# Kernel optimization log

Hardware: AMD Instinct MI355X
Metric: run time of the kernel (lower is better)

Reference implementation:

```python
import jax, jax.numpy as jnp
import numpy as np

N, F, FE = 50000, 128, 1
E, EI, G = 800000, 400000, 64
NEG_SLOPE = 0.01


def _linear_params(key, out_dim, in_dim):
    k1, k2 = jax.random.split(key)
    bound = 1.0 / np.sqrt(in_dim)
    w = jax.random.uniform(k1, (out_dim, in_dim), jnp.float32, -bound, bound)
    b = jax.random.uniform(k2, (out_dim,), jnp.float32, -bound, bound)
    return w, b


def setup_inputs() -> dict:
    key = jax.random.key(0)
    ks = jax.random.split(key, 16)
    inp = {
        'x': jax.random.normal(ks[0], (N, F), jnp.float32),
        'edge_index': jax.random.randint(ks[1], (2, E), 0, N, jnp.int64) if jax.config.read('jax_enable_x64') else jax.random.randint(ks[1], (2, E), 0, N, jnp.int32),
        'edge_attr': jax.random.normal(ks[2], (E, FE), jnp.float32),
        'internal_edge_index': jax.random.randint(ks[3], (2, EI), 0, N, jnp.int32),
        'internal_edge_attr': jax.random.normal(ks[4], (EI, FE), jnp.float32),
        'batch': jnp.sort(jax.random.randint(ks[5], (N,), 0, G, jnp.int32)),
    }
    # four conv sub-modules: message Linear(2F+FE -> 1), update Linear(F+1 -> F)
    names = ['e1', 'e2', 'i1', 'i2']
    for i, nm in enumerate(names):
        wm, bm = _linear_params(ks[6 + i], 1, 2 * F + FE)
        wu, bu = _linear_params(ks[10 + i], F, F + 1)
        inp[f'wm_{nm}'], inp[f'bm_{nm}'] = wm, bm
        inp[f'wu_{nm}'], inp[f'bu_{nm}'] = wu, bu
    inp['fc1_w'], inp['fc1_b'] = _linear_params(ks[14], 128, 2 * F)
    inp['fc2_w'], inp['fc2_b'] = _linear_params(ks[15], 1, 128)
    return inp


def _conv(x, edge_index, edge_attr, wm, bm, wu, bu):
    s, d = edge_index[0], edge_index[1]
    # gather + tiny linear: [E, 2F+FE] @ [2F+FE, 1]
    msg_in = jnp.concatenate([x[s], x[d], edge_attr], axis=1)
    msg = msg_in @ wm.T + bm                      # [E, 1]
    msg = jax.nn.leaky_relu(msg, NEG_SLOPE)
    msg = jax.nn.softmax(msg, axis=1)             # [E,1] -> all ones (faithful)
    node_msg = jax.ops.segment_sum(msg, s, num_segments=x.shape[0])  # [N, 1]
    upd = jnp.concatenate([x, node_msg], axis=1) @ wu.T + bu          # [N, F]
    upd = jax.nn.leaky_relu(upd, NEG_SLOPE)
    return jax.nn.softmax(upd, axis=1)


def _scatter_mean(x, seg, num_segments):
    s = jax.ops.segment_sum(x, seg, num_segments=num_segments)
    c = jax.ops.segment_sum(jnp.ones((x.shape[0], 1), x.dtype), seg, num_segments=num_segments)
    return s / jnp.maximum(c, 1.0)


def reference(x, edge_index, edge_attr, internal_edge_index, internal_edge_attr, batch,
              wm_e1, bm_e1, wu_e1, bu_e1, wm_e2, bm_e2, wu_e2, bu_e2,
              wm_i1, bm_i1, wu_i1, bu_i1, wm_i2, bm_i2, wu_i2, bu_i2,
              fc1_w, fc1_b, fc2_w, fc2_b):
    ext = _conv(x, edge_index, edge_attr, wm_e1, bm_e1, wu_e1, bu_e1)
    ext = _conv(ext, edge_index, edge_attr, wm_e2, bm_e2, wu_e2, bu_e2)
    itn = _conv(x, internal_edge_index, internal_edge_attr, wm_i1, bm_i1, wu_i1, bu_i1)
    itn = _conv(itn, internal_edge_index, internal_edge_attr, wm_i2, bm_i2, wu_i2, bu_i2)
    ez = _scatter_mean(ext, batch, G)             # [G, F]
    iz = _scatter_mean(itn, batch, G)             # [G, F]
    z = jnp.concatenate([ez, iz], axis=1)         # [G, 2F]
    z = jax.nn.relu(z @ fc1_w.T + fc1_b)
    return z @ fc2_w.T + fc2_b                    # [G, 1]
```

## Files before the change

kernel.cpp:

```cpp
#include <hip/hip_runtime.h>
#include <hip/hip_bf16.h>

#define NN  50000
#define FD  128
#define NE  800000
#define NEI 400000
#define NG  64

#define EZ_STRIDE  8192
#define CNT_SLOTS  13
#define DEGB_WORDS 12544

#define HB_E 32
#define HB_I 16
#define HB_SLICE 6250

#define AB_BAT 13
#define AB_PRE 8
#define AB_ZERO 8

typedef short  short8 __attribute__((ext_vector_type(8)));
typedef float  f32x4  __attribute__((ext_vector_type(4)));

union S8 { short8 s; unsigned int u[4]; };

__device__ __forceinline__ unsigned short bf16h(float f) {
  unsigned int u = __float_as_uint(f);
  u += 0x7FFFu + ((u >> 16) & 1u);
  return (unsigned short)(u >> 16);
}
__device__ __forceinline__ float bf16tof(unsigned short h) {
  return __uint_as_float(((unsigned int)h) << 16);
}
__device__ __forceinline__ unsigned int pk_bf16(float a, float b) {
  __hip_bfloat162 h = __float22bfloat162_rn(make_float2(a, b));
  unsigned int u;
  __builtin_memcpy(&u, &h, 4);
  return u;
}
__device__ __forceinline__ float frcp(float x) { return __builtin_amdgcn_rcpf(x); }

__global__ __launch_bounds__(256) void aux_kernel(
    const int4* __restrict__ ei4, const int4* __restrict__ iei4,
    const int* __restrict__ batch,
    const float* __restrict__ wu_e1, const float* __restrict__ wu_e2,
    const float* __restrict__ wu_i1, const float* __restrict__ wu_i2,
    unsigned int* __restrict__ degp,
    int* __restrict__ cnt,
    unsigned short* __restrict__ WB, float* __restrict__ wcolp,
    int4* __restrict__ zbuf, int zquads)
{
  __shared__ __align__(16) unsigned char SM[DEGB_WORDS * 4];
  __shared__ int hb[64];
  unsigned int* H  = (unsigned int*)SM;
  float*        WS = (float*)SM;
  const int b = blockIdx.x, t = threadIdx.x;

  if (b < HB_E + HB_I) {
    for (int i = t; i < DEGB_WORDS; i += 256) H[i] = 0;
    __syncthreads();
    if (b < HB_E) {
      const int beg = b * HB_SLICE;
      const int end = min(beg + HB_SLICE, NE / 4);
      for (int i = beg + t; i < end; i += 256) {
        const int4 v = ei4[i];
        atomicAdd(&H[v.x >> 2], 1u << (8 * (v.x & 3)));
        atomicAdd(&H[v.y >> 2], 1u << (8 * (v.y & 3)));
        atomicAdd(&H[v.z >> 2], 1u << (8 * (v.z & 3)));
        atomicAdd(&H[v.w >> 2], 1u << (8 * (v.w & 3)));
      }
    } else {
      const int beg = (b - HB_E) * HB_SLICE;
      const int end = min(beg + HB_SLICE, NEI / 4);
      for (int i = beg + t; i < end; i += 256) {
        const int4 v = iei4[i];
        atomicAdd(&H[v.x >> 2], 1u << (8 * (v.x & 3)));
        atomicAdd(&H[v.y >> 2], 1u << (8 * (v.y & 3)));
        atomicAdd(&H[v.z >> 2], 1u << (8 * (v.z & 3)));
        atomicAdd(&H[v.w >> 2], 1u << (8 * (v.w & 3)));
      }
    }
    __syncthreads();
    unsigned int* dst = degp + (size_t)b * DEGB_WORDS;
    for (int i = t; i < DEGB_WORDS; i += 256) dst[i] = H[i];
  } else if (b < HB_E + HB_I + AB_BAT) {
    const int ib = b - HB_E - HB_I;
    if (t < 64) hb[t] = 0;
    __syncthreads();
    const int base = ib * 4096 + t;
    for (int u = 0; u < 16; ++u) {
      const int i = base + u * 256;
      if (i < NN) atomicAdd(&hb[batch[i]], 1);
    }
    __syncthreads();
    if (t < 64) cnt[ib * 64 + t] = hb[t];
  } else if (b < HB_E + HB_I + AB_BAT + AB_PRE) {
    const int pb = b - HB_E - HB_I - AB_BAT;
    const int c  = pb >> 1;
    const int h  = pb & 1;
    const float* wu = (c == 0) ? wu_e1 : (c == 1) ? wu_e2 : (c == 2) ? wu_i1 : wu_i2;
    for (int idx = t; idx < 64 * 129; idx += 256)
      WS[idx] = wu[(size_t)h * 64 * 129 + idx];
    __syncthreads();
    const int lane = t & 63, u = t >> 6;
    const int n = lane & 15, quad = lane >> 4;
    const int ct = 4 * h + u;
    unsigned short* wb = WB + c * 32768;
    #pragma unroll
    for (int kc = 0; kc < 4; ++kc) {
      const int k0 = kc * 32 + quad * 8;
      const float* src = &WS[(u * 16 + n) * 129 + k0];
      short8 hi, lo;
      #pragma unroll
      for (int e = 0; e < 8; ++e) {
        const float v = src[e];
        const unsigned short hh = bf16h(v);
        hi[e] = (short)hh;
        lo[e] = (short)bf16h(v - bf16tof(hh));
      }
      const int fbase = ((ct * 4 + kc) * 2) * 512 + lane * 8;
      *(short8*)&wb[fbase]       = hi;
      *(short8*)&wb[fbase + 512] = lo;
    }
    if (t < 64) wcolp[c * 128 + h * 64 + t] = WS[t * 129 + 128];
  } else {
    const int zb = b - HB_E - HB_I - AB_BAT - AB_PRE;
    for (int i = zb * 256 + t; i < zquads; i += AB_ZERO * 256)
      zbuf[i] = make_int4(0, 0, 0, 0);
  }
}

#define ROWS 32

__global__ __launch_bounds__(256, 4) void conv_mfma_kernel(
    const float* __restrict__ x,
    const unsigned int* __restrict__ degp,
    const int* __restrict__ batch,
    const unsigned short* __restrict__ WB, const float* __restrict__ wcolp,
    const float* __restrict__ bu_e1, const float* __restrict__ bu_e2,
    const float* __restrict__ bu_i1, const float* __restrict__ bu_i2,
    float* __restrict__ ez_sum, float* __restrict__ iz_sum, int ncopy)
{
  __shared__ unsigned short XT[2][4096];
  __shared__ float degsE[ROWS];
  __shared__ float degsI[ROWS];
  __shared__ int   bg[ROWS];
  __shared__ float redA[ROWS * 4];
  __shared__ float redB[ROWS * 4];

  const int tid  = threadIdx.x;
  const int lane = tid & 63;
  const int w    = tid >> 6;
  const int n    = lane & 15;
  const int q    = lane >> 4;
  const int mbase = blockIdx.x * ROWS;
  const int cp = blockIdx.x & (ncopy - 1);
  const int jA = w * 16 + n;
  const int jB = (w + 4) * 16 + n;

#define LOADP(C, KC, P) do {                                                  \
    const unsigned short* _p = WB + (C) * 32768 + (w * 4 + (KC)) * 1024 + lane * 8; \
    P[0] = *(const short8*)&_p[0];     P[1] = *(const short8*)&_p[512];       \
    P[2] = *(const short8*)&_p[16384]; P[3] = *(const short8*)&_p[16896];     \
  } while (0)

#define PSTEP(XB, KC, P, ACC) do {                                            \
    _Pragma("unroll")                                                          \
    for (int rt = 0; rt < 2; ++rt) {                                           \
      const short8 Ah = *(const short8*)&XT[XB][((rt * 4 + (KC)) * 64 + lane) * 8]; \
      f32x4 c0 = ACC[rt][0];                                                   \
      c0 = __builtin_amdgcn_mfma_f32_16x16x32_bf16(Ah, P[0], c0, 0, 0, 0);     \
      c0 = __builtin_amdgcn_mfma_f32_16x16x32_bf16(Ah, P[1], c0, 0, 0, 0);     \
      ACC[rt][0] = c0;                                                         \
      f32x4 c1 = ACC[rt][1];                                                   \
      c1 = __builtin_amdgcn_mfma_f32_16x16x32_bf16(Ah, P[2], c1, 0, 0, 0);     \
      c1 = __builtin_amdgcn_mfma_f32_16x16x32_bf16(Ah, P[3], c1, 0, 0, 0);     \
      ACC[rt][1] = c1;                                                         \
    }                                                                          \
  } while (0)

#define PASS(XB, C, ACC) do {                                                 \
    PSTEP(XB, 0, Pa, ACC);                                                    \
    LOADP(C, 2, Pa);                                                          \
    PSTEP(XB, 1, Pb, ACC);                                                    \
    LOADP(C, 3, Pb);                                                          \
    PSTEP(XB, 2, Pa, ACC);                                                    \
    PSTEP(XB, 3, Pb, ACC);                                                    \
  } while (0)

  short8 Pa[4], Pb[4];
  LOADP(0, 0, Pa);
  LOADP(0, 1, Pb);
  const float wcE1A = wcolp[0 * 128 + jA], wcE1B = wcolp[0 * 128 + jB];
  const float wcE2A = wcolp[1 * 128 + jA], wcE2B = wcolp[1 * 128 + jB];
  const float wcI1A = wcolp[2 * 128 + jA], wcI1B = wcolp[2 * 128 + jB];
  const float wcI2A = wcolp[3 * 128 + jA], wcI2B = wcolp[3 * 128 + jB];
  const float bE1A = bu_e1[jA], bE1B = bu_e1[jB];
  const float bE2A = bu_e2[jA], bE2B = bu_e2[jB];
  const float bI1A = bu_i1[jA], bI1B = bu_i1[jB];
  const float bI2A = bu_i2[jA], bI2B = bu_i2[jB];

  #pragma unroll
  for (int u = 0; u < 2; ++u) {
    const int oct  = u * 256 + tid;
    const int frag = oct >> 6, l = oct & 63;
    const int row  = (frag >> 2) * 16 + (l & 15);
    const int k0   = (frag & 3) * 32 + (l >> 4) * 8;
    const int node = mbase + row;
    float4 a = make_float4(0.f, 0.f, 0.f, 0.f), bb = a;
    if (node < NN) {
      const float* xr = x + (size_t)node * FD + k0;
      a  = *(const float4*)xr;
      bb = *(const float4*)(xr + 4);
    }
    S8 hi;
    hi.u[0] = pk_bf16(a.x, a.y);
    hi.u[1] = pk_bf16(a.z, a.w);
    hi.u[2] = pk_bf16(bb.x, bb.y);
    hi.u[3] = pk_bf16(bb.z, bb.w);
    *(short8*)&XT[0][oct * 8] = hi.s;
  }
  {
    const int node = tid >> 3, c = tid & 7;
    const int gn = mbase + node;
    const bool v = gn < NN;
    const int nc = v ? gn : (NN - 1);
    const int wrd = nc >> 2, sh = 8 * (nc & 3);
    unsigned pe = 0, pi = 0;
    #pragma unroll
    for (int k = 0; k < 4; ++k)
      pe += (degp[(size_t)(c + 8 * k) * DEGB_WORDS + wrd] >> sh) & 255u;
    #pragma unroll
    for (int k = 0; k < 2; ++k)
      pi += (degp[(size_t)(HB_E + c + 8 * k) * DEGB_WORDS + wrd] >> sh) & 255u;
    float fe = (float)pe, fi = (float)pi;
    #pragma unroll
    for (int s = 1; s < 8; s <<= 1) { fe += __shfl_xor(fe, s); fi += __shfl_xor(fi, s); }
    if (c == 0) {
      degsE[node] = v ? fe : 0.f;
      degsI[node] = v ? fi : 0.f;
      bg[node]    = batch[nc];
    }
  }
  __syncthreads();

  f32x4 aE[2][2], aI[2][2];
  #pragma unroll
  for (int rt = 0; rt < 2; ++rt)
    #pragma unroll
    for (int s = 0; s < 2; ++s) {
      aE[rt][s] = (f32x4){0.f, 0.f, 0.f, 0.f};
      aI[rt][s] = (f32x4){0.f, 0.f, 0.f, 0.f};
    }
  PASS(0, 0, aE);
  LOADP(2, 0, Pa);
  LOADP(2, 1, Pb);
  PASS(0, 2, aI);

  #pragma unroll
  for (int rt = 0; rt < 2; ++rt) {
    const float4 dE = *(const float4*)&degsE[rt * 16 + 4 * q];
    const float4 dI = *(const float4*)&degsI[rt * 16 + 4 * q];
    const float dEv[4] = {dE.x, dE.y, dE.z, dE.w};
    const float dIv[4] = {dI.x, dI.y, dI.z, dI.w};
    #pragma unroll
    for (int r = 0; r < 4; ++r) {
      float v;
      v = aE[rt][0][r] + bE1A + dEv[r] * wcE1A; v = fmaxf(v, 0.01f * v); aE[rt][0][r] = __expf(v);
      v = aE[rt][1][r] + bE1B + dEv[r] * wcE1B; v = fmaxf(v, 0.01f * v); aE[rt][1][r] = __expf(v);
      v = aI[rt][0][r] + bI1A + dIv[r] * wcI1A; v = fmaxf(v, 0.01f * v); aI[rt][0][r] = __expf(v);
      v = aI[rt][1][r] + bI1B + dIv[r] * wcI1B; v = fmaxf(v, 0.01f * v); aI[rt][1][r] = __expf(v);
    }
  }

  #pragma unroll
  for (int rt = 0; rt < 2; ++rt) {
    #pragma unroll
    for (int r = 0; r < 4; ++r) {
      float te = aE[rt][0][r] + aE[rt][1][r];
      float ti = aI[rt][0][r] + aI[rt][1][r];
      te += __shfl_xor(te, 1); ti += __shfl_xor(ti, 1);
      te += __shfl_xor(te, 2); ti += __shfl_xor(ti, 2);
      te += __shfl_xor(te, 4); ti += __shfl_xor(ti, 4);
      te += __shfl_xor(te, 8); ti += __shfl_xor(ti, 8);
      if (n == 0) {
        redA[(rt * 16 + q * 4 + r) * 4 + w] = te;
        redB[(rt * 16 + q * 4 + r) * 4 + w] = ti;
      }
    }
  }

  unsigned int pE[2][2][2], pI[2][2][2];
  #pragma unroll
  for (int rt = 0; rt < 2; ++rt)
    #pragma unroll
    for (int s = 0; s < 2; ++s) {
      pE[rt][s][0] = pk_bf16(aE[rt][s][0], aE[rt][s][1]);
      pE[rt][s][1] = pk_bf16(aE[rt][s][2], aE[rt][s][3]);
      pI[rt][s][0] = pk_bf16(aI[rt][s][0], aI[rt][s][1]);
      pI[rt][s][1] = pk_bf16(aI[rt][s][2], aI[rt][s][3]);
    }
  LOADP(1, 0, Pa);
  LOADP(1, 1, Pb);

  #pragma unroll
  for (int rt = 0; rt < 2; ++rt)
    #pragma unroll
    for (int s = 0; s < 2; ++s) {
      const int ct = w + s * 4;
      const int ib = ((rt * 4 + (ct >> 1)) * 64 + ((ct & 1) * 2 + (n >> 3)) * 16 + q * 4) * 8 + (n & 7);
      XT[1][ib]      = (unsigned short)(pE[rt][s][0] & 0xFFFFu);
      XT[1][ib + 8]  = (unsigned short)(pE[rt][s][0] >> 16);
      XT[1][ib + 16] = (unsigned short)(pE[rt][s][1] & 0xFFFFu);
      XT[1][ib + 24] = (unsigned short)(pE[rt][s][1] >> 16);
    }
  __syncthreads();

  #pragma unroll
  for (int rt = 0; rt < 2; ++rt)
    #pragma unroll
    for (int s = 0; s < 2; ++s) {
      const int ct = w + s * 4;
      const int ib = ((rt * 4 + (ct >> 1)) * 64 + ((ct & 1) * 2 + (n >> 3)) * 16 + q * 4) * 8 + (n & 7);
      XT[0][ib]      = (unsigned short)(pI[rt][s][0] & 0xFFFFu);
      XT[0][ib + 8]  = (unsigned short)(pI[rt][s][0] >> 16);
      XT[0][ib + 16] = (unsigned short)(pI[rt][s][1] & 0xFFFFu);
      XT[0][ib + 24] = (unsigned short)(pI[rt][s][1] >> 16);
    }

  float s1iE, s1iI;
  {
    const int rl = (lane & 31) * 4;
    const f32x4 a0 = *(const f32x4*)&redA[rl];
    s1iE = frcp((a0[0] + a0[1]) + (a0[2] + a0[3]));
    const f32x4 b0 = *(const f32x4*)&redB[rl];
    s1iI = frcp((b0[0] + b0[1]) + (b0[2] + b0[3]));
  }

  f32x4 cE[2][2], cI[2][2];
  #pragma unroll
  for (int rt = 0; rt < 2; ++rt)
    #pragma unroll
    for (int s = 0; s < 2; ++s) cE[rt][s] = (f32x4){0.f, 0.f, 0.f, 0.f};
  PASS(1, 1, cE);
  LOADP(3, 0, Pa);
  LOADP(3, 1, Pb);
  __syncthreads();

  #pragma unroll
  for (int rt = 0; rt < 2; ++rt)
    #pragma unroll
    for (int s = 0; s < 2; ++s) cI[rt][s] = (f32x4){0.f, 0.f, 0.f, 0.f};
  PASS(0, 3, cI);

  #pragma unroll
  for (int rt = 0; rt < 2; ++rt) {
    const float4 dE = *(const float4*)&degsE[rt * 16 + 4 * q];
    const float4 dI = *(const float4*)&degsI[rt * 16 + 4 * q];
    const float dEv[4] = {dE.x, dE.y, dE.z, dE.w};
    const float dIv[4] = {dI.x, dI.y, dI.z, dI.w};
    #pragma unroll
    for (int r = 0; r < 4; ++r) {
      const int row = rt * 16 + q * 4 + r;
      const float i1e = __shfl(s1iE, row);
      const float i1i = __shfl(s1iI, row);
      float v;
      v = cE[rt][0][r] * i1e + bE2A + dEv[r] * wcE2A; v = fmaxf(v, 0.01f * v); cE[rt][0][r] = __expf(v);
      v = cE[rt][1][r] * i1e + bE2B + dEv[r] * wcE2B; v = fmaxf(v, 0.01f * v); cE[rt][1][r] = __expf(v);
      v = cI[rt][0][r] * i1i + bI2A + dIv[r] * wcI2A; v = fmaxf(v, 0.01f * v); cI[rt][0][r] = __expf(v);
      v = cI[rt][1][r] * i1i + bI2B + dIv[r] * wcI2B; v = fmaxf(v, 0.01f * v); cI[rt][1][r] = __expf(v);
    }
    #pragma unroll
    for (int r = 0; r < 4; ++r) {
      float te = cE[rt][0][r] + cE[rt][1][r];
      float ti = cI[rt][0][r] + cI[rt][1][r];
      te += __shfl_xor(te, 1); ti += __shfl_xor(ti, 1);
      te += __shfl_xor(te, 2); ti += __shfl_xor(ti, 2);
      te += __shfl_xor(te, 4); ti += __shfl_xor(ti, 4);
      te += __shfl_xor(te, 8); ti += __shfl_xor(ti, 8);
      if (n == 0) {
        redA[(rt * 16 + q * 4 + r) * 4 + w] = te;
        redB[(rt * 16 + q * 4 + r) * 4 + w] = ti;
      }
    }
  }
  __syncthreads();

  float s2iE, s2iI;
  {
    const int rl = (lane & 31) * 4;
    const f32x4 a0 = *(const f32x4*)&redA[rl];
    s2iE = frcp((a0[0] + a0[1]) + (a0[2] + a0[3]));
    const f32x4 b0 = *(const f32x4*)&redB[rl];
    s2iI = frcp((b0[0] + b0[1]) + (b0[2] + b0[3]));
  }
  #pragma unroll
  for (int rt = 0; rt < 2; ++rt) {
    #pragma unroll
    for (int r = 0; r < 4; ++r) {
      const int row = rt * 16 + q * 4 + r;
      const float i2e = __shfl(s2iE, row);
      const float i2i = __shfl(s2iI, row);
      cE[rt][0][r] *= i2e; cE[rt][1][r] *= i2e;
      cI[rt][0][r] *= i2i; cI[rt][1][r] *= i2i;
    }
  }

  {
    float* __restrict__ ezp = ez_sum + (size_t)cp * EZ_STRIDE;
    float* __restrict__ izp = iz_sum + (size_t)cp * EZ_STRIDE;

    if (mbase + ROWS - 1 >= NN) {
      #pragma unroll
      for (int rt = 0; rt < 2; ++rt)
        #pragma unroll
        for (int r = 0; r < 4; ++r) {
          const int row = rt * 16 + q * 4 + r;
          if (mbase + row >= NN) {
            cE[rt][0][r] = 0.f; cE[rt][1][r] = 0.f;
            cI[rt][0][r] = 0.f; cI[rt][1][r] = 0.f;
          }
        }
    }

    const int g0 = bg[0], g1 = bg[ROWS - 1];
    for (int g = g0; g <= g1; ++g) {
      const bool one = (g0 == g1);
      float seA = 0.f, siA = 0.f, seB = 0.f, siB = 0.f;
      #pragma unroll
      for (int rt = 0; rt < 2; ++rt)
        #pragma unroll
        for (int r = 0; r < 4; ++r) {
          const int row = rt * 16 + q * 4 + r;
          const bool m = one || (bg[row] == g);
          seA += m ? cE[rt][0][r] : 0.f;
          seB += m ? cE[rt][1][r] : 0.f;
          siA += m ? cI[rt][0][r] : 0.f;
          siB += m ? cI[rt][1][r] : 0.f;
        }
      seA += __shfl_xor(seA, 16); siA += __shfl_xor(siA, 16);
      seB += __shfl_xor(seB, 16); siB += __shfl_xor(siB, 16);
      seA += __shfl_xor(seA, 32); siA += __shfl_xor(siA, 32);
      seB += __shfl_xor(seB, 32); siB += __shfl_xor(siB, 32);
      if (q == 0) {
        atomicAdd(&ezp[g * FD + jA], seA);
        atomicAdd(&ezp[g * FD + jB], seB);
        atomicAdd(&izp[g * FD + jA], siA);
        atomicAdd(&izp[g * FD + jB], siB);
      }
    }
  }
#undef LOADP
#undef PSTEP
#undef PASS
}

__global__ __launch_bounds__(128) void fc_kernel(
    const float* __restrict__ ez_sum, const float* __restrict__ iz_sum,
    const int* __restrict__ cnt,
    const float* __restrict__ fc1_w, const float* __restrict__ fc1_b,
    const float* __restrict__ fc2_w, const float* __restrict__ fc2_b,
    float* __restrict__ out, int ncopy)
{
  __shared__ float z[256];
  __shared__ float red2[2];
  const int g = blockIdx.x, t = threadIdx.x;
  int cc = 0;
  #pragma unroll
  for (int c = 0; c < CNT_SLOTS; ++c) cc += cnt[c * 64 + g];
  float se = 0.f, si = 0.f;
  for (int c = 0; c < ncopy; ++c) {
    se += ez_sum[(size_t)c * EZ_STRIDE + g * 128 + t];
    si += iz_sum[(size_t)c * EZ_STRIDE + g * 128 + t];
  }
  const float denom = fmaxf((float)cc, 1.0f);
  z[t]       = se / denom;
  z[128 + t] = si / denom;
  __syncthreads();

  const float* wr = fc1_w + (size_t)t * 256;
  float a = fc1_b[t];
  #pragma unroll 4
  for (int c = 0; c < 256; c += 4) {
    const float4 wv = *(const float4*)(wr + c);
    a += wv.x * z[c] + wv.y * z[c + 1] + wv.z * z[c + 2] + wv.w * z[c + 3];
  }
  a = fmaxf(a, 0.f) * fc2_w[t];
  a += __shfl_xor(a, 1);
  a += __shfl_xor(a, 2);
  a += __shfl_xor(a, 4);
  a += __shfl_xor(a, 8);
  a += __shfl_xor(a, 16);
  a += __shfl_xor(a, 32);
  if ((t & 63) == 0) red2[t >> 6] = a;
  __syncthreads();
  if (t == 0) out[g] = red2[0] + red2[1] + fc2_b[0];
}

extern "C" void kernel_launch(void* const* d_in, const int* in_sizes, int n_in,
                              void* d_out, int out_size, void* d_ws, size_t ws_size,
                              hipStream_t stream) {
  const float* x     = (const float*)d_in[0];
  const int4*  ei4   = (const int4*) d_in[1];
  const int4*  iei4  = (const int4*) d_in[3];
  const int*   batch = (const int*)  d_in[5];
  const float* wu_e1 = (const float*)d_in[8];
  const float* bu_e1 = (const float*)d_in[9];
  const float* wu_e2 = (const float*)d_in[12];
  const float* bu_e2 = (const float*)d_in[13];
  const float* wu_i1 = (const float*)d_in[16];
  const float* bu_i1 = (const float*)d_in[17];
  const float* wu_i2 = (const float*)d_in[20];
  const float* bu_i2 = (const float*)d_in[21];
  const float* fc1_w = (const float*)d_in[22];
  const float* fc1_b = (const float*)d_in[23];
  const float* fc2_w = (const float*)d_in[24];
  const float* fc2_b = (const float*)d_in[25];

  const size_t need8 = 8ull * 2 * 32768 + CNT_SLOTS * 256 + 262144 + 2048
                     + (size_t)(HB_E + HB_I) * DEGB_WORDS * 4;
  const int ncopy = (ws_size >= need8) ? 8 : 1;

  char* ws = (char*)d_ws;
  size_t off = 0;
  float* ez      = (float*)(ws + off); off += (size_t)ncopy * 32768;
  float* iz      = (float*)(ws + off); off += (size_t)ncopy * 32768;
  const int zquads = (int)(((size_t)ncopy * 2 * 32768) / 16);
  int*   cnt     = (int*)(ws + off);  off += CNT_SLOTS * 256;
  unsigned short* WB = (unsigned short*)(ws + off); off += 262144;
  float* wcolp   = (float*)(ws + off); off += 2048;
  unsigned int* degp = (unsigned int*)(ws + off);
  off += (size_t)(HB_E + HB_I) * DEGB_WORDS * 4;

  aux_kernel<<<HB_E + HB_I + AB_BAT + AB_PRE + AB_ZERO, 256, 0, stream>>>(
      ei4, iei4, batch, wu_e1, wu_e2, wu_i1, wu_i2,
      degp, cnt, WB, wcolp, (int4*)ez, zquads);

  conv_mfma_kernel<<<dim3((NN + ROWS - 1) / ROWS), 256, 0, stream>>>(
      x, degp, batch, WB, wcolp,
      bu_e1, bu_e2, bu_i1, bu_i2, ez, iz, ncopy);

  fc_kernel<<<NG, 128, 0, stream>>>(ez, iz, cnt, fc1_w, fc1_b, fc2_w, fc2_b,
                                    (float*)d_out, ncopy);
}
```

Before: 170.2 us.

## Split external and internal conv chains across a second grid dimension

The conv kernel used to run both the external and the internal two-layer conv chains in every block. It now launches twice as many blocks, with blockIdx.y selecting one chain per block. This halves the per-block register and accumulator footprint and doubles the available parallelism, which should improve occupancy and latency hiding. The cost is that each block loads and converts the x tile a second time, and the batch/degree metadata is read twice overall.

```diff
diff --git a/kernel.cpp b/kernel.cpp
--- a/kernel.cpp
+++ b/kernel.cpp
@@ -142,8 +142,7 @@
     float* __restrict__ ez_sum, float* __restrict__ iz_sum, int ncopy)
 {
   __shared__ unsigned short XT[2][4096];
-  __shared__ float degsE[ROWS];
-  __shared__ float degsI[ROWS];
+  __shared__ float degs[ROWS];
   __shared__ int   bg[ROWS];
   __shared__ float redA[ROWS * 4];
   __shared__ float redB[ROWS * 4];
@@ -154,9 +153,16 @@
   const int n    = lane & 15;
   const int q    = lane >> 4;
   const int mbase = blockIdx.x * ROWS;
+  const int chain = blockIdx.y;
   const int cp = blockIdx.x & (ncopy - 1);
   const int jA = w * 16 + n;
   const int jB = (w + 4) * 16 + n;
+
+  const int c1 = chain * 2;
+  const int c2 = chain * 2 + 1;
+  const float* bu1 = chain ? bu_i1 : bu_e1;
+  const float* bu2 = chain ? bu_i2 : bu_e2;
+  float* __restrict__ gsum = chain ? iz_sum : ez_sum;
 
 #define LOADP(C, KC, P) do {                                                  \
     const unsigned short* _p = WB + (C) * 32768 + (w * 4 + (KC)) * 1024 + lane * 8; \
@@ -172,10 +178,10 @@
       c0 = __builtin_amdgcn_mfma_f32_16x16x32_bf16(Ah, P[0], c0, 0, 0, 0);     \
       c0 = __builtin_amdgcn_mfma_f32_16x16x32_bf16(Ah, P[1], c0, 0, 0, 0);     \
       ACC[rt][0] = c0;                                                         \
-      f32x4 c1 = ACC[rt][1];                                                   \
-      c1 = __builtin_amdgcn_mfma_f32_16x16x32_bf16(Ah, P[2], c1, 0, 0, 0);     \
-      c1 = __builtin_amdgcn_mfma_f32_16x16x32_bf16(Ah, P[3], c1, 0, 0, 0);     \
-      ACC[rt][1] = c1;                                                         \
+      f32x4 c1v = ACC[rt][1];                                                  \
+      c1v = __builtin_amdgcn_mfma_f32_16x16x32_bf16(Ah, P[2], c1v, 0, 0, 0);   \
+      c1v = __builtin_amdgcn_mfma_f32_16x16x32_bf16(Ah, P[3], c1v, 0, 0, 0);   \
+      ACC[rt][1] = c1v;                                                        \
     }                                                                          \
   } while (0)
 
@@ -189,16 +195,12 @@
   } while (0)
 
   short8 Pa[4], Pb[4];
-  LOADP(0, 0, Pa);
-  LOADP(0, 1, Pb);
-  const float wcE1A = wcolp[0 * 128 + jA], wcE1B = wcolp[0 * 128 + jB];
-  const float wcE2A = wcolp[1 * 128 + jA], wcE2B = wcolp[1 * 128 + jB];
-  const float wcI1A = wcolp[2 * 128 + jA], wcI1B = wcolp[2 * 128 + jB];
-  const float wcI2A = wcolp[3 * 128 + jA], wcI2B = wcolp[3 * 128 + jB];
-  const float bE1A = bu_e1[jA], bE1B = bu_e1[jB];
-  const float bE2A = bu_e2[jA], bE2B = bu_e2[jB];
-  const float bI1A = bu_i1[jA], bI1B = bu_i1[jB];
-  const float bI2A = bu_i2[jA], bI2B = bu_i2[jB];
+  LOADP(c1, 0, Pa);
+  LOADP(c1, 1, Pb);
+  const float wc1A = wcolp[c1 * 128 + jA], wc1B = wcolp[c1 * 128 + jB];
+  const float wc2A = wcolp[c2 * 128 + jA], wc2B = wcolp[c2 * 128 + jB];
+  const float b1A = bu1[jA], b1B = bu1[jB];
+  const float b2A = bu2[jA], b2B = bu2[jB];
 
   #pragma unroll
   for (int u = 0; u < 2; ++u) {
@@ -226,50 +228,37 @@
     const bool v = gn < NN;
     const int nc = v ? gn : (NN - 1);
     const int wrd = nc >> 2, sh = 8 * (nc & 3);
-    unsigned pe = 0, pi = 0;
-    #pragma unroll
-    for (int k = 0; k < 4; ++k)
-      pe += (degp[(size_t)(c + 8 * k) * DEGB_WORDS + wrd] >> sh) & 255u;
-    #pragma unroll
-    for (int k = 0; k < 2; ++k)
-      pi += (degp[(size_t)(HB_E + c + 8 * k) * DEGB_WORDS + wrd] >> sh) & 255u;
-    float fe = (float)pe, fi = (float)pi;
-    #pragma unroll
-    for (int s = 1; s < 8; s <<= 1) { fe += __shfl_xor(fe, s); fi += __shfl_xor(fi, s); }
+    const unsigned int* dp = degp + (chain ? (size_t)HB_E * DEGB_WORDS : 0);
+    const int ncop = chain ? HB_I : HB_E;
+    unsigned p = 0;
+    for (int cc = c; cc < ncop; cc += 8)
+      p += (dp[(size_t)cc * DEGB_WORDS + wrd] >> sh) & 255u;
+    float f = (float)p;
+    #pragma unroll
+    for (int s = 1; s < 8; s <<= 1) f += __shfl_xor(f, s);
     if (c == 0) {
-      degsE[node] = v ? fe : 0.f;
-      degsI[node] = v ? fi : 0.f;
-      bg[node]    = batch[nc];
+      degs[node] = v ? f : 0.f;
+      bg[node]   = batch[nc];
     }
   }
   __syncthreads();
 
-  f32x4 aE[2][2], aI[2][2];
+  f32x4 a1[2][2];
   #pragma unroll
   for (int rt = 0; rt < 2; ++rt)
     #pragma unroll
-    for (int s = 0; s < 2; ++s) {
-      aE[rt][s] = (f32x4){0.f, 0.f, 0.f, 0.f};
-      aI[rt][s] = (f32x4){0.f, 0.f, 0.f, 0.f};
-    }
-  PASS(0, 0, aE);
-  LOADP(2, 0, Pa);
-  LOADP(2, 1, Pb);
-  PASS(0, 2, aI);
+    for (int s = 0; s < 2; ++s) a1[rt][s] = (f32x4){0.f, 0.f, 0.f, 0.f};
+  PASS(0, c1, a1);
 
   #pragma unroll
   for (int rt = 0; rt < 2; ++rt) {
-    const float4 dE = *(const float4*)&degsE[rt * 16 + 4 * q];
-    const float4 dI = *(const float4*)&degsI[rt * 16 + 4 * q];
-    const float dEv[4] = {dE.x, dE.y, dE.z, dE.w};
-    const float dIv[4] = {dI.x, dI.y, dI.z, dI.w};
+    const float4 dg = *(const float4*)&degs[rt * 16 + 4 * q];
+    const float dv[4] = {dg.x, dg.y, dg.z, dg.w};
     #pragma unroll
     for (int r = 0; r < 4; ++r) {
       float v;
-      v = aE[rt][0][r] + bE1A + dEv[r] * wcE1A; v = fmaxf(v, 0.01f * v); aE[rt][0][r] = __expf(v);
-      v = aE[rt][1][r] + bE1B + dEv[r] * wcE1B; v = fmaxf(v, 0.01f * v); aE[rt][1][r] = __expf(v);
-      v = aI[rt][0][r] + bI1A + dIv[r] * wcI1A; v = fmaxf(v, 0.01f * v); aI[rt][0][r] = __expf(v);
-      v = aI[rt][1][r] + bI1B + dIv[r] * wcI1B; v = fmaxf(v, 0.01f * v); aI[rt][1][r] = __expf(v);
+      v = a1[rt][0][r] + b1A + dv[r] * wc1A; v = fmaxf(v, 0.01f * v); a1[rt][0][r] = __expf(v);
+      v = a1[rt][1][r] + b1B + dv[r] * wc1B; v = fmaxf(v, 0.01f * v); a1[rt][1][r] = __expf(v);
     }
   }
 
@@ -277,31 +266,25 @@
   for (int rt = 0; rt < 2; ++rt) {
     #pragma unroll
     for (int r = 0; r < 4; ++r) {
-      float te = aE[rt][0][r] + aE[rt][1][r];
-      float ti = aI[rt][0][r] + aI[rt][1][r];
-      te += __shfl_xor(te, 1); ti += __shfl_xor(ti, 1);
-      te += __shfl_xor(te, 2); ti += __shfl_xor(ti, 2);
-      te += __shfl_xor(te, 4); ti += __shfl_xor(ti, 4);
-      te += __shfl_xor(te, 8); ti += __shfl_xor(ti, 8);
-      if (n == 0) {
-        redA[(rt * 16 + q * 4 + r) * 4 + w] = te;
-        redB[(rt * 16 + q * 4 + r) * 4 + w] = ti;
-      }
-    }
-  }
-
-  unsigned int pE[2][2][2], pI[2][2][2];
+      float te = a1[rt][0][r] + a1[rt][1][r];
+      te += __shfl_xor(te, 1);
+      te += __shfl_xor(te, 2);
+      te += __shfl_xor(te, 4);
+      te += __shfl_xor(te, 8);
+      if (n == 0) redA[(rt * 16 + q * 4 + r) * 4 + w] = te;
+    }
+  }
+
+  unsigned int pk[2][2][2];
   #pragma unroll
   for (int rt = 0; rt < 2; ++rt)
     #pragma unroll
     for (int s = 0; s < 2; ++s) {
-      pE[rt][s][0] = pk_bf16(aE[rt][s][0], aE[rt][s][1]);
-      pE[rt][s][1] = pk_bf16(aE[rt][s][2], aE[rt][s][3]);
-      pI[rt][s][0] = pk_bf16(aI[rt][s][0], aI[rt][s][1]);
-      pI[rt][s][1] = pk_bf16(aI[rt][s][2], aI[rt][s][3]);
-    }
-  LOADP(1, 0, Pa);
-  LOADP(1, 1, Pb);
+      pk[rt][s][0] = pk_bf16(a1[rt][s][0], a1[rt][s][1]);
+      pk[rt][s][1] = pk_bf16(a1[rt][s][2], a1[rt][s][3]);
+    }
+  LOADP(c2, 0, Pa);
+  LOADP(c2, 1, Pb);
 
   #pragma unroll
   for (int rt = 0; rt < 2; ++rt)
@@ -309,106 +292,70 @@
     for (int s = 0; s < 2; ++s) {
       const int ct = w + s * 4;
       const int ib = ((rt * 4 + (ct >> 1)) * 64 + ((ct & 1) * 2 + (n >> 3)) * 16 + q * 4) * 8 + (n & 7);
-      XT[1][ib]      = (unsigned short)(pE[rt][s][0] & 0xFFFFu);
-      XT[1][ib + 8]  = (unsigned short)(pE[rt][s][0] >> 16);
-      XT[1][ib + 16] = (unsigned short)(pE[rt][s][1] & 0xFFFFu);
-      XT[1][ib + 24] = (unsigned short)(pE[rt][s][1] >> 16);
+      XT[1][ib]      = (unsigned short)(pk[rt][s][0] & 0xFFFFu);
+      XT[1][ib + 8]  = (unsigned short)(pk[rt][s][0] >> 16);
+      XT[1][ib + 16] = (unsigned short)(pk[rt][s][1] & 0xFFFFu);
+      XT[1][ib + 24] = (unsigned short)(pk[rt][s][1] >> 16);
     }
   __syncthreads();
 
-  #pragma unroll
-  for (int rt = 0; rt < 2; ++rt)
-    #pragma unroll
-    for (int s = 0; s < 2; ++s) {
-      const int ct = w + s * 4;
-      const int ib = ((rt * 4 + (ct >> 1)) * 64 + ((ct & 1) * 2 + (n >> 3)) * 16 + q * 4) * 8 + (n & 7);
-      XT[0][ib]      = (unsigned short)(pI[rt][s][0] & 0xFFFFu);
-      XT[0][ib + 8]  = (unsigned short)(pI[rt][s][0] >> 16);
-      XT[0][ib + 16] = (unsigned short)(pI[rt][s][1] & 0xFFFFu);
-      XT[0][ib + 24] = (unsigned short)(pI[rt][s][1] >> 16);
-    }
-
-  float s1iE, s1iI;
+  float s1i;
   {
     const int rl = (lane & 31) * 4;
     const f32x4 a0 = *(const f32x4*)&redA[rl];
-    s1iE = frcp((a0[0] + a0[1]) + (a0[2] + a0[3]));
-    const f32x4 b0 = *(const f32x4*)&redB[rl];
-    s1iI = frcp((b0[0] + b0[1]) + (b0[2] + b0[3]));
-  }
-
-  f32x4 cE[2][2], cI[2][2];
+    s1i = frcp((a0[0] + a0[1]) + (a0[2] + a0[3]));
+  }
+
+  f32x4 a2[2][2];
   #pragma unroll
   for (int rt = 0; rt < 2; ++rt)
     #pragma unroll
-    for (int s = 0; s < 2; ++s) cE[rt][s] = (f32x4){0.f, 0.f, 0.f, 0.f};
-  PASS(1, 1, cE);
-  LOADP(3, 0, Pa);
-  LOADP(3, 1, Pb);
-  __syncthreads();
-
-  #pragma unroll
-  for (int rt = 0; rt < 2; ++rt)
-    #pragma unroll
-    for (int s = 0; s < 2; ++s) cI[rt][s] = (f32x4){0.f, 0.f, 0.f, 0.f};
-  PASS(0, 3, cI);
+    for (int s = 0; s < 2; ++s) a2[rt][s] = (f32x4){0.f, 0.f, 0.f, 0.f};
+  PASS(1, c2, a2);
 
   #pragma unroll
   for (int rt = 0; rt < 2; ++rt) {
-    const float4 dE = *(const float4*)&degsE[rt * 16 + 4 * q];
-    const float4 dI = *(const float4*)&degsI[rt * 16 + 4 * q];
-    const float dEv[4] = {dE.x, dE.y, dE.z, dE.w};
-    const float dIv[4] = {dI.x, dI.y, dI.z, dI.w};
+    const float4 dg = *(const float4*)&degs[rt * 16 + 4 * q];
+    const float dv[4] = {dg.x, dg.y, dg.z, dg.w};
     #pragma unroll
     for (int r = 0; r < 4; ++r) {
       const int row = rt * 16 + q * 4 + r;
-      const float i1e = __shfl(s1iE, row);
-      const float i1i = __shfl(s1iI, row);
+      const float i1 = __shfl(s1i, row);
       float v;
-      v = cE[rt][0][r] * i1e + bE2A + dEv[r] * wcE2A; v = fmaxf(v, 0.01f * v); cE[rt][0][r] = __expf(v);
-      v = cE[rt][1][r] * i1e + bE2B + dEv[r] * wcE2B; v = fmaxf(v, 0.01f * v); cE[rt][1][r] = __expf(v);
-      v = cI[rt][0][r] * i1i + bI2A + dIv[r] * wcI2A; v = fmaxf(v, 0.01f * v); cI[rt][0][r] = __expf(v);
-      v = cI[rt][1][r] * i1i + bI2B + dIv[r] * wcI2B; v = fmaxf(v, 0.01f * v); cI[rt][1][r] = __expf(v);
+      v = a2[rt][0][r] * i1 + b2A + dv[r] * wc2A; v = fmaxf(v, 0.01f * v); a2[rt][0][r] = __expf(v);
+      v = a2[rt][1][r] * i1 + b2B + dv[r] * wc2B; v = fmaxf(v, 0.01f * v); a2[rt][1][r] = __expf(v);
     }
     #pragma unroll
     for (int r = 0; r < 4; ++r) {
-      float te = cE[rt][0][r] + cE[rt][1][r];
-      float ti = cI[rt][0][r] + cI[rt][1][r];
-      te += __shfl_xor(te, 1); ti += __shfl_xor(ti, 1);
-      te += __shfl_xor(te, 2); ti += __shfl_xor(ti, 2);
-      te += __shfl_xor(te, 4); ti += __shfl_xor(ti, 4);
-      te += __shfl_xor(te, 8); ti += __shfl_xor(ti, 8);
-      if (n == 0) {
-        redA[(rt * 16 + q * 4 + r) * 4 + w] = te;
-        redB[(rt * 16 + q * 4 + r) * 4 + w] = ti;
-      }
+      float te = a2[rt][0][r] + a2[rt][1][r];
+      te += __shfl_xor(te, 1);
+      te += __shfl_xor(te, 2);
+      te += __shfl_xor(te, 4);
+      te += __shfl_xor(te, 8);
+      if (n == 0) redB[(rt * 16 + q * 4 + r) * 4 + w] = te;
     }
   }
   __syncthreads();
 
-  float s2iE, s2iI;
+  float s2i;
   {
     const int rl = (lane & 31) * 4;
-    const f32x4 a0 = *(const f32x4*)&redA[rl];
-    s2iE = frcp((a0[0] + a0[1]) + (a0[2] + a0[3]));
     const f32x4 b0 = *(const f32x4*)&redB[rl];
-    s2iI = frcp((b0[0] + b0[1]) + (b0[2] + b0[3]));
+    s2i = frcp((b0[0] + b0[1]) + (b0[2] + b0[3]));
   }
   #pragma unroll
   for (int rt = 0; rt < 2; ++rt) {
     #pragma unroll
     for (int r = 0; r < 4; ++r) {
       const int row = rt * 16 + q * 4 + r;
-      const float i2e = __shfl(s2iE, row);
-      const float i2i = __shfl(s2iI, row);
-      cE[rt][0][r] *= i2e; cE[rt][1][r] *= i2e;
-      cI[rt][0][r] *= i2i; cI[rt][1][r] *= i2i;
+      const float i2 = __shfl(s2i, row);
+      a2[rt][0][r] *= i2;
+      a2[rt][1][r] *= i2;
     }
   }
 
   {
-    float* __restrict__ ezp = ez_sum + (size_t)cp * EZ_STRIDE;
-    float* __restrict__ izp = iz_sum + (size_t)cp * EZ_STRIDE;
+    float* __restrict__ gp = gsum + (size_t)cp * EZ_STRIDE;
 
     if (mbase + ROWS - 1 >= NN) {
       #pragma unroll
@@ -416,37 +363,28 @@
         #pragma unroll
         for (int r = 0; r < 4; ++r) {
           const int row = rt * 16 + q * 4 + r;
-          if (mbase + row >= NN) {
-            cE[rt][0][r] = 0.f; cE[rt][1][r] = 0.f;
-            cI[rt][0][r] = 0.f; cI[rt][1][r] = 0.f;
-          }
+          if (mbase + row >= NN) { a2[rt][0][r] = 0.f; a2[rt][1][r] = 0.f; }
         }
     }
 
     const int g0 = bg[0], g1 = bg[ROWS - 1];
     for (int g = g0; g <= g1; ++g) {
       const bool one = (g0 == g1);
-      float seA = 0.f, siA = 0.f, seB = 0.f, siB = 0.f;
+      float sA = 0.f, sB = 0.f;
       #pragma unroll
       for (int rt = 0; rt < 2; ++rt)
         #pragma unroll
         for (int r = 0; r < 4; ++r) {
           const int row = rt * 16 + q * 4 + r;
           const bool m = one || (bg[row] == g);
-          seA += m ? cE[rt][0][r] : 0.f;
-          seB += m ? cE[rt][1][r] : 0.f;
-          siA += m ? cI[rt][0][r] : 0.f;
-          siB += m ? cI[rt][1][r] : 0.f;
+          sA += m ? a2[rt][0][r] : 0.f;
+          sB += m ? a2[rt][1][r] : 0.f;
         }
-      seA += __shfl_xor(seA, 16); siA += __shfl_xor(siA, 16);
-      seB += __shfl_xor(seB, 16); siB += __shfl_xor(siB, 16);
-      seA += __shfl_xor(seA, 32); siA += __shfl_xor(siA, 32);
-      seB += __shfl_xor(seB, 32); siB += __shfl_xor(siB, 32);
+      sA += __shfl_xor(sA, 16); sB += __shfl_xor(sB, 16);
+      sA += __shfl_xor(sA, 32); sB += __shfl_xor(sB, 32);
       if (q == 0) {
-        atomicAdd(&ezp[g * FD + jA], seA);
-        atomicAdd(&ezp[g * FD + jB], seB);
-        atomicAdd(&izp[g * FD + jA], siA);
-        atomicAdd(&izp[g * FD + jB], siB);
+        atomicAdd(&gp[g * FD + jA], sA);
+        atomicAdd(&gp[g * FD + jB], sB);
       }
     }
   }
@@ -536,7 +474,7 @@
       ei4, iei4, batch, wu_e1, wu_e2, wu_i1, wu_i2,
       degp, cnt, WB, wcolp, (int4*)ez, zquads);
 
-  conv_mfma_kernel<<<dim3((NN + ROWS - 1) / ROWS), 256, 0, stream>>>(
+  conv_mfma_kernel<<<dim3((NN + ROWS - 1) / ROWS, 2), 256, 0, stream>>>(
       x, degp, batch, WB, wcolp,
       bu_e1, bu_e2, bu_i1, bu_i2, ez, iz, ncopy);
 
```

Result: no change. 171.2 us (+0.6%).
